# Kernel tuning notes

Measured on AMD Instinct MI355X. Metric: run time of the kernel, lower is better.

## Reference

```python
import jax, jax.numpy as jnp
import numpy as np

L = 2          # n_layer
H = 8          # n_head
DM = 512       # d_model
DFF = 2048     # d_ff
DH = DM // H   # head dim (query_dimensions)
M = DH         # Favor n_dims random features
B, S = 1, 2048
EPS = 1e-6     # causal linear attention eps
LN_EPS = 1e-5  # torch LayerNorm default


def setup_inputs() -> dict:
    key = jax.random.key(0)
    ks = jax.random.split(key, 12)
    sc = 0.02
    d = {}
    d['x'] = jax.random.normal(ks[0], (B, S, DM), dtype=jnp.float32)
    for i, (n, shape) in enumerate([('Wq', (L, DM, DM)), ('Wk', (L, DM, DM)),
                                    ('Wv', (L, DM, DM)), ('Wo', (L, DM, DM)),
                                    ('W1', (L, DM, DFF)), ('W2', (L, DFF, DM))]):
        d[n] = jax.random.normal(ks[i + 1], shape, dtype=jnp.float32) * sc
    d['bq'] = jnp.zeros((L, DM), jnp.float32)
    d['bk'] = jnp.zeros((L, DM), jnp.float32)
    d['bv'] = jnp.zeros((L, DM), jnp.float32)
    d['bo'] = jnp.zeros((L, DM), jnp.float32)
    d['b1'] = jnp.zeros((L, DFF), jnp.float32)
    d['b2'] = jnp.zeros((L, DM), jnp.float32)
    d['g1'] = jnp.ones((L, DM), jnp.float32)
    d['be1'] = jnp.zeros((L, DM), jnp.float32)
    d['g2'] = jnp.ones((L, DM), jnp.float32)
    d['be2'] = jnp.zeros((L, DM), jnp.float32)
    # FAVOR+ random projection matrix per layer: [Dh, M]
    d['omega'] = jax.random.normal(ks[7], (L, DH, M), dtype=jnp.float32)
    return d


def _favor(x, omega):
    # x: [B,S,H,Dh]; softmax_temp = 1/sqrt(Dh) applied as x * sqrt(temp)
    xs = x * (DH ** -0.25)
    nrm = jnp.sum(xs * xs, axis=-1, keepdims=True)       # [B,S,H,1]
    u = jnp.einsum('bshd,dm->bshm', xs, omega)           # [B,S,H,M]
    return jnp.exp(u - 0.5 * nrm) * (M ** -0.5)


def _ln(x, g, b):
    mu = jnp.mean(x, -1, keepdims=True)
    var = jnp.mean((x - mu) ** 2, -1, keepdims=True)
    return (x - mu) * jax.lax.rsqrt(var + LN_EPS) * g + b


def _forward(x, Wq, bq, Wk, bk, Wv, bv, Wo, bo, omega,
             W1, b1, W2, b2, g1, be1, g2, be2):
    out = x
    for l in range(L):
        q = (out @ Wq[l] + bq[l]).reshape(B, S, H, DH)
        k = (out @ Wk[l] + bk[l]).reshape(B, S, H, DH)
        v = (out @ Wv[l] + bv[l]).reshape(B, S, H, DH)
        pq = _favor(q, omega[l])
        pk = _favor(k, omega[l])
        # causal linear attention: running sums of phi(k) v^T and phi(k)
        kv = jnp.cumsum(jnp.einsum('bshm,bshd->bshmd', pk, v), axis=1)  # [B,S,H,M,Dh]
        num = jnp.einsum('bshm,bshmd->bshd', pq, kv)
        den = jnp.einsum('bshm,bshm->bsh', pq, jnp.cumsum(pk, axis=1)) + EPS
        a = (num / den[..., None]).reshape(B, S, DM)
        # post-norm encoder layer (fast-transformers TransformerEncoderLayer)
        out = out + (a @ Wo[l] + bo[l])
        out = _ln(out, g1[l], be1[l])
        y = jax.nn.relu(out @ W1[l] + b1[l]) @ W2[l] + b2[l]
        out = _ln(out + y, g2[l], be2[l])
    return out


def reference(x, Wq, bq, Wk, bk, Wv, bv, Wo, bo, omega,
              W1, b1, W2, b2, g1, be1, g2, be2):
    return _forward(x, Wq, bq, Wk, bk, Wv, bv, Wo, bo, omega,
                    W1, b1, W2, b2, g1, be1, g2, be2)
```

## Files before the change

### kernel.cpp

```cpp
#include <hip/hip_runtime.h>
#include <hip/hip_bf16.h>

#define S_  2048
#define DM_ 512
#define H_  8
#define DH_ 64
#define MF_ 64
#define DFF_ 2048
#define L_  2
#define CT_ 64
#define NC_ (S_ / CT_)
#define EPS_ 1e-6f
#define LN_EPS_ 1e-5f

#define LSW_   3145728
#define W1OFF_ 1048576
#define W2OFF_ 2097152
#define WOOFF_ 786432

typedef unsigned short ushortT;
typedef unsigned int u32;
typedef float f4 __attribute__((ext_vector_type(4)));
typedef short s8 __attribute__((ext_vector_type(8)));
typedef u32 u32x2 __attribute__((ext_vector_type(2)));

__device__ __forceinline__ ushortT f2b(float f) {
  union { float f; unsigned u; } v; v.f = f;
  unsigned r = v.u + 0x7fffu + ((v.u >> 16) & 1u);
  return (ushortT)(r >> 16);
}
__device__ __forceinline__ float bu2f(ushortT h) {
  union { unsigned u; float f; } v; v.u = ((unsigned)h) << 16; return v.f;
}
__device__ __forceinline__ u32 pk2(float a, float b) {
  return (u32)f2b(a) | ((u32)f2b(b) << 16);
}

__global__ __launch_bounds__(256) void tcast_all(
    const float* __restrict__ x,
    const float* __restrict__ Wq, const float* __restrict__ Wk,
    const float* __restrict__ Wv, const float* __restrict__ Wo,
    const float* __restrict__ W1, const float* __restrict__ W2,
    const float* __restrict__ omg,
    float* __restrict__ cur, ushortT* __restrict__ curb,
    ushortT* __restrict__ wb, ushortT* __restrict__ omgTb) {
  const int bid = blockIdx.x;
  const int t = threadIdx.x;
  if (bid >= 6152) {
    const int i = (bid - 6152) * 256 + t;
    float v = x[i];
    cur[i] = v;
    curb[i] = f2b(v);
    return;
  }
  __shared__ ushortT tile[32][33];
  const float* src; ushortT* dst; int K, N, bx, by;
  if (bid < 2048) {
    const int z = bid >> 8, widx = z & 3, lay = z >> 2;
    const float* s4[4] = {Wq, Wk, Wv, Wo};
    src = s4[widx] + (size_t)lay * DM_ * DM_;
    dst = wb + (size_t)lay * LSW_ + (size_t)widx * DM_ * DM_;
    K = DM_; N = DM_; bx = bid & 15; by = (bid >> 4) & 15;
  } else if (bid < 4096) {
    const int r = bid - 2048;
    const int lay = r >> 10;
    src = W1 + (size_t)lay * DM_ * DFF_;
    dst = wb + (size_t)lay * LSW_ + W1OFF_;
    K = DM_; N = DFF_; bx = r & 63; by = (r >> 6) & 15;
  } else if (bid < 6144) {
    const int r = bid - 4096;
    const int lay = r >> 10;
    src = W2 + (size_t)lay * DFF_ * DM_;
    dst = wb + (size_t)lay * LSW_ + W2OFF_;
    K = DFF_; N = DM_; bx = r & 15; by = (r >> 4) & 63;
  } else {
    const int r = bid - 6144;
    const int lay = r >> 2;
    src = omg + (size_t)lay * DH_ * MF_;
    dst = omgTb + (size_t)lay * DH_ * MF_;
    K = DH_; N = MF_; bx = r & 1; by = (r >> 1) & 1;
  }
  const int cc = t & 31, r0 = t >> 5;
  const int n0 = bx * 32, k0 = by * 32;
#pragma unroll
  for (int i = 0; i < 4; ++i) {
    int r = r0 + 8 * i;
    tile[r][cc] = f2b(src[(size_t)(k0 + r) * N + n0 + cc]);
  }
  __syncthreads();
#pragma unroll
  for (int i = 0; i < 4; ++i) {
    int r = r0 + 8 * i;
    dst[(size_t)(n0 + r) * K + k0 + cc] = tile[cc][r];
  }
}

template<bool OUT_BF16>
__global__ __launch_bounds__(256) void mgemm(
    const ushortT* __restrict__ A, const ushortT* __restrict__ Wt,
    const float* __restrict__ bq_, const float* __restrict__ bk_,
    const float* __restrict__ bv_,
    float* __restrict__ Cf, ushortT* __restrict__ Cb, int K, int N) {
  __shared__ ushortT sA[2][2048];
  __shared__ ushortT sB[2][2048];
  const int t = threadIdx.x;
  const int w = t >> 6, l = t & 63;
  const int wm = w >> 1, wn = w & 1;
  const int n0 = blockIdx.x * 64, m0 = blockIdx.y * 64;
  const int z = blockIdx.z;
  const ushortT* Wz = Wt + (size_t)z * K * N;
  const float* bias = (z == 0) ? bq_ : (z == 1 ? bk_ : bv_);

  const int rs = w * 16 + (l >> 2);
  const int qs = (l & 3) ^ ((rs >> 1) & 3);
  const ushortT* gA = A  + (size_t)(m0 + rs) * K + qs * 8;
  const ushortT* gB = Wz + (size_t)(n0 + rs) * K + qs * 8;

  const int Ra = wm * 32 + (l & 15);
  const int Rb = wn * 32 + (l & 15);
  const int qq = l >> 4;
  const int aoff = (Ra * 4 + (qq ^ ((Ra >> 1) & 3))) * 8;
  const int boff = (Rb * 4 + (qq ^ ((Rb >> 1) & 3))) * 8;

  f4 acc[2][2];
#pragma unroll
  for (int i = 0; i < 2; ++i)
#pragma unroll
    for (int j = 0; j < 2; ++j) acc[i][j] = (f4){0.f, 0.f, 0.f, 0.f};

  auto stage = [&](int buf, int ko) {
    __builtin_amdgcn_global_load_lds(
        (const __attribute__((address_space(1))) void*)(gA + ko),
        (__attribute__((address_space(3))) void*)(&sA[buf][w * 512]), 16, 0, 0);
    __builtin_amdgcn_global_load_lds(
        (const __attribute__((address_space(1))) void*)(gB + ko),
        (__attribute__((address_space(3))) void*)(&sB[buf][w * 512]), 16, 0, 0);
  };

  stage(0, 0);
  const int nk = K >> 5;
  for (int ks = 0; ks < nk; ++ks) {
    __syncthreads();
    if (ks + 1 < nk) stage((ks + 1) & 1, (ks + 1) * 32);
    const ushortT* pa = sA[ks & 1];
    const ushortT* pb = sB[ks & 1];
    s8 a0 = *(const s8*)(pa + aoff);
    s8 a1 = *(const s8*)(pa + aoff + 512);
    s8 b0 = *(const s8*)(pb + boff);
    s8 b1 = *(const s8*)(pb + boff + 512);
    acc[0][0] = __builtin_amdgcn_mfma_f32_16x16x32_bf16(a0, b0, acc[0][0], 0, 0, 0);
    acc[0][1] = __builtin_amdgcn_mfma_f32_16x16x32_bf16(a0, b1, acc[0][1], 0, 0, 0);
    acc[1][0] = __builtin_amdgcn_mfma_f32_16x16x32_bf16(a1, b0, acc[1][0], 0, 0, 0);
    acc[1][1] = __builtin_amdgcn_mfma_f32_16x16x32_bf16(a1, b1, acc[1][1], 0, 0, 0);
  }

  const size_t outz = (size_t)z * S_ * N;
  const int colb = n0 + wn * 32 + (l & 15);
  const int rowb = m0 + wm * 32 + ((l >> 4) << 2);
#pragma unroll
  for (int mt = 0; mt < 2; ++mt) {
#pragma unroll
    for (int nt = 0; nt < 2; ++nt) {
      const int c = colb + nt * 16;
      const float bv = bias[c];
#pragma unroll
      for (int r = 0; r < 4; ++r) {
        const int rr = rowb + mt * 16 + r;
        float v = acc[mt][nt][r] + bv;
        if (OUT_BF16) Cb[outz + (size_t)rr * N + c] = f2b(v);
        else          Cf[outz + (size_t)rr * N + c] = v;
      }
    }
  }
}

__global__ __launch_bounds__(256) void mgemm_part(
    const ushortT* __restrict__ A, const ushortT* __restrict__ Wt,
    float* __restrict__ PS, int K, int N, int KS) {
  __shared__ ushortT sA[2][2048];
  __shared__ ushortT sB[2][2048];
  const int t = threadIdx.x;
  const int w = t >> 6, l = t & 63;
  const int wm = w >> 1, wn = w & 1;
  const int n0 = blockIdx.x * 64, m0 = blockIdx.y * 64;
  const int z = blockIdx.z;

  const int rs = w * 16 + (l >> 2);
  const int qs = (l & 3) ^ ((rs >> 1) & 3);
  const ushortT* gA = A  + (size_t)(m0 + rs) * K + z * KS + qs * 8;
  const ushortT* gB = Wt + (size_t)(n0 + rs) * K + z * KS + qs * 8;

  const int Ra = wm * 32 + (l & 15);
  const int Rb = wn * 32 + (l & 15);
  const int qq = l >> 4;
  const int aoff = (Ra * 4 + (qq ^ ((Ra >> 1) & 3))) * 8;
  const int boff = (Rb * 4 + (qq ^ ((Rb >> 1) & 3))) * 8;

  f4 acc[2][2];
#pragma unroll
  for (int i = 0; i < 2; ++i)
#pragma unroll
    for (int j = 0; j < 2; ++j) acc[i][j] = (f4){0.f, 0.f, 0.f, 0.f};

  auto stage = [&](int buf, int ko) {
    __builtin_amdgcn_global_load_lds(
        (const __attribute__((address_space(1))) void*)(gA + ko),
        (__attribute__((address_space(3))) void*)(&sA[buf][w * 512]), 16, 0, 0);
    __builtin_amdgcn_global_load_lds(
        (const __attribute__((address_space(1))) void*)(gB + ko),
        (__attribute__((address_space(3))) void*)(&sB[buf][w * 512]), 16, 0, 0);
  };

  stage(0, 0);
  const int nk = KS >> 5;
  for (int ks = 0; ks < nk; ++ks) {
    __syncthreads();
    if (ks + 1 < nk) stage((ks + 1) & 1, (ks + 1) * 32);
    const ushortT* pa = sA[ks & 1];
    const ushortT* pb = sB[ks & 1];
    s8 a0 = *(const s8*)(pa + aoff);
    s8 a1 = *(const s8*)(pa + aoff + 512);
    s8 b0 = *(const s8*)(pb + boff);
    s8 b1 = *(const s8*)(pb + boff + 512);
    acc[0][0] = __builtin_amdgcn_mfma_f32_16x16x32_bf16(a0, b0, acc[0][0], 0, 0, 0);
    acc[0][1] = __builtin_amdgcn_mfma_f32_16x16x32_bf16(a0, b1, acc[0][1], 0, 0, 0);
    acc[1][0] = __builtin_amdgcn_mfma_f32_16x16x32_bf16(a1, b0, acc[1][0], 0, 0, 0);
    acc[1][1] = __builtin_amdgcn_mfma_f32_16x16x32_bf16(a1, b1, acc[1][1], 0, 0, 0);
  }

  float* out = PS + (size_t)z * S_ * N;
  const int colb = n0 + wn * 32 + (l & 15);
  const int rowb = m0 + wm * 32 + ((l >> 4) << 2);
#pragma unroll
  for (int mt = 0; mt < 2; ++mt) {
#pragma unroll
    for (int nt = 0; nt < 2; ++nt) {
      const int c = colb + nt * 16;
#pragma unroll
      for (int r = 0; r < 4; ++r)
        out[(size_t)(rowb + mt * 16 + r) * N + c] = acc[mt][nt][r];
    }
  }
}

template<bool FULL>
__global__ __launch_bounds__(256) void mgemm128(
    const ushortT* __restrict__ A, const ushortT* __restrict__ Wt,
    const float* __restrict__ bias, float* __restrict__ PS,
    ushortT* __restrict__ Cb, int K, int N, int KS) {
  __shared__ ushortT sA[2][4096];
  __shared__ ushortT sB[2][4096];
  const int t = threadIdx.x;
  const int w = t >> 6, l = t & 63, lr = l & 15, q = l >> 4;
  const int wm = w >> 1, wn = w & 1;
  const int n0 = blockIdx.x * 128, m0 = blockIdx.y * 128;
  const int z = blockIdx.z;

  const int s0 = w * 128 + l, s1 = s0 + 64;
  const int r0 = s0 >> 2, kq0 = (s0 & 3) ^ ((r0 >> 1) & 3);
  const int r1 = s1 >> 2, kq1 = (s1 & 3) ^ ((r1 >> 1) & 3);
  const ushortT* gA0 = A  + (size_t)(m0 + r0) * K + z * KS + kq0 * 8;
  const ushortT* gA1 = A  + (size_t)(m0 + r1) * K + z * KS + kq1 * 8;
  const ushortT* gB0 = Wt + (size_t)(n0 + r0) * K + z * KS + kq0 * 8;
  const ushortT* gB1 = Wt + (size_t)(n0 + r1) * K + z * KS + kq1 * 8;

  int aoff[4], boff[4];
#pragma unroll
  for (int i = 0; i < 4; ++i) {
    const int RA = wm * 64 + i * 16 + lr;
    const int RB = wn * 64 + i * 16 + lr;
    aoff[i] = (RA * 4 + (q ^ ((RA >> 1) & 3))) * 8;
    boff[i] = (RB * 4 + (q ^ ((RB >> 1) & 3))) * 8;
  }

  f4 acc[4][4];
#pragma unroll
  for (int i = 0; i < 4; ++i)
#pragma unroll
    for (int j = 0; j < 4; ++j) acc[i][j] = (f4){0.f, 0.f, 0.f, 0.f};

  auto stage = [&](int buf, int ko) {
    __builtin_amdgcn_global_load_lds(
        (const __attribute__((address_space(1))) void*)(gA0 + ko),
        (__attribute__((address_space(3))) void*)(&sA[buf][w * 1024]), 16, 0, 0);
    __builtin_amdgcn_global_load_lds(
        (const __attribute__((address_space(1))) void*)(gA1 + ko),
        (__attribute__((address_space(3))) void*)(&sA[buf][w * 1024 + 512]), 16, 0, 0);
    __builtin_amdgcn_global_load_lds(
        (const __attribute__((address_space(1))) void*)(gB0 + ko),
        (__attribute__((address_space(3))) void*)(&sB[buf][w * 1024]), 16, 0, 0);
    __builtin_amdgcn_global_load_lds(
        (const __attribute__((address_space(1))) void*)(gB1 + ko),
        (__attribute__((address_space(3))) void*)(&sB[buf][w * 1024 + 512]), 16, 0, 0);
  };

  stage(0, 0);
  const int nk = (FULL ? K : KS) >> 5;
  for (int ks = 0; ks < nk; ++ks) {
    __syncthreads();
    if (ks + 1 < nk) stage((ks + 1) & 1, (ks + 1) * 32);
    const ushortT* pa = sA[ks & 1];
    const ushortT* pb = sB[ks & 1];
    s8 a[4], b[4];
#pragma unroll
    for (int i = 0; i < 4; ++i) {
      a[i] = *(const s8*)(pa + aoff[i]);
      b[i] = *(const s8*)(pb + boff[i]);
    }
#pragma unroll
    for (int mt = 0; mt < 4; ++mt)
#pragma unroll
      for (int nt = 0; nt < 4; ++nt)
        acc[mt][nt] = __builtin_amdgcn_mfma_f32_16x16x32_bf16(a[mt], b[nt], acc[mt][nt], 0, 0, 0);
  }

  const int colb = n0 + wn * 64 + lr;
  const int rowb = m0 + wm * 64 + q * 4;
  if (FULL) {
#pragma unroll
    for (int nt = 0; nt < 4; ++nt) {
      const int c = colb + nt * 16;
      const float bv = bias[c];
#pragma unroll
      for (int mt = 0; mt < 4; ++mt) {
#pragma unroll
        for (int r = 0; r < 4; ++r) {
          const int rr = rowb + mt * 16 + r;
          Cb[(size_t)rr * N + c] = f2b(fmaxf(acc[mt][nt][r] + bv, 0.f));
        }
      }
    }
  } else {
    float* out = PS + (size_t)z * S_ * N;
#pragma unroll
    for (int mt = 0; mt < 4; ++mt)
#pragma unroll
      for (int nt = 0; nt < 4; ++nt) {
        const int c = colb + nt * 16;
#pragma unroll
        for (int r = 0; r < 4; ++r)
          out[(size_t)(rowb + mt * 16 + r) * N + c] = acc[mt][nt][r];
      }
  }
}

__global__ __launch_bounds__(256) void redln(const float* __restrict__ PS, int nsplit,
                                             const float* __restrict__ bias,
                                             const float* __restrict__ res,
                                             const float* __restrict__ g,
                                             const float* __restrict__ be,
                                             float* __restrict__ outF,
                                             ushortT* __restrict__ outB) {
  const int s = blockIdx.x, t = threadIdx.x;
  float v0 = bias[t] + res[(size_t)s * DM_ + t];
  float v1 = bias[t + 256] + res[(size_t)s * DM_ + 256 + t];
  for (int z = 0; z < nsplit; ++z) {
    const float* p = PS + (size_t)z * S_ * DM_ + (size_t)s * DM_;
    v0 += p[t];
    v1 += p[256 + t];
  }
  float sum = v0 + v1, sq = v0 * v0 + v1 * v1;
  for (int off = 32; off > 0; off >>= 1) {
    sum += __shfl_down(sum, off);
    sq += __shfl_down(sq, off);
  }
  __shared__ float ssum[4], ssq[4];
  __shared__ float smean, srstd;
  const int w = t >> 6;
  if ((t & 63) == 0) { ssum[w] = sum; ssq[w] = sq; }
  __syncthreads();
  if (t == 0) {
    float S1 = ssum[0] + ssum[1] + ssum[2] + ssum[3];
    float S2 = ssq[0] + ssq[1] + ssq[2] + ssq[3];
    float mu = S1 / DM_;
    smean = mu;
    srstd = rsqrtf(S2 / DM_ - mu * mu + LN_EPS_);
  }
  __syncthreads();
  const float mu = smean, rs = srstd;
  float o0 = (v0 - mu) * rs * g[t] + be[t];
  float o1 = (v1 - mu) * rs * g[256 + t] + be[256 + t];
  outF[(size_t)s * DM_ + t] = o0;
  outF[(size_t)s * DM_ + 256 + t] = o1;
  if (outB) {
    outB[(size_t)s * DM_ + t] = f2b(o0);
    outB[(size_t)s * DM_ + 256 + t] = f2b(o1);
  }
}

__global__ __launch_bounds__(256) void favor_cs(const ushortT* __restrict__ qkv,
                                                const ushortT* __restrict__ omgT,
                                                ushortT* __restrict__ PQb,
                                                ushortT* __restrict__ PKb,
                                                float* __restrict__ KVcT,
                                                float* __restrict__ Kc) {
  const int c = blockIdx.x, h = blockIdx.y, t = threadIdx.x;
  const int w = t >> 6, l = t & 63, lr = l & 15, q = l >> 4;
  __shared__ ushortT xq[64 * 72], xk[64 * 72], vT[64 * 72], omT[64 * 72];
  __shared__ ushortT pq[64 * 72], pk[64 * 72], pkT[64 * 72];
  __shared__ float nrm[128];

  const ushortT* qg = qkv + (size_t)(c * CT_) * DM_ + h * DH_;
  const ushortT* kg = qg + (size_t)S_ * DM_;
  const ushortT* vg = kg + (size_t)S_ * DM_;

  for (int i = t; i < 512; i += 256) {
    const int s = i >> 3, seg = i & 7;
    *(s8*)&xq[s * 72 + seg * 8] = *(const s8*)(qg + (size_t)s * DM_ + seg * 8);
    *(s8*)&xk[s * 72 + seg * 8] = *(const s8*)(kg + (size_t)s * DM_ + seg * 8);
    s8 av = *(const s8*)(vg + (size_t)s * DM_ + seg * 8);
#pragma unroll
    for (int j = 0; j < 8; ++j) vT[(seg * 8 + j) * 72 + s] = (ushortT)av[j];
    *(s8*)&omT[s * 72 + seg * 8] = *(const s8*)(omgT + s * 64 + seg * 8);
  }
  __syncthreads();

  if (t < 128) {
    const ushortT* src = (t < 64) ? xq : xk;
    const int s = t & 63;
    float a = 0.f;
#pragma unroll
    for (int seg = 0; seg < 8; ++seg) {
      s8 vv = *(const s8*)(src + s * 72 + seg * 8);
#pragma unroll
      for (int j = 0; j < 8; ++j) {
        float f = bu2f((ushortT)vv[j]);
        a += f * f;
      }
    }
    nrm[t] = a;
  }
  __syncthreads();

  {
    const float gam = 0.35355339059327373f;
    const int s0 = w * 16;
    s8 aq0 = *(const s8*)&xq[(s0 + lr) * 72 + q * 8];
    s8 aq1 = *(const s8*)&xq[(s0 + lr) * 72 + 32 + q * 8];
    s8 ak0 = *(const s8*)&xk[(s0 + lr) * 72 + q * 8];
    s8 ak1 = *(const s8*)&xk[(s0 + lr) * 72 + 32 + q * 8];
#pragma unroll
    for (int mt = 0; mt < 4; ++mt) {
      s8 b0 = *(const s8*)&omT[(mt * 16 + lr) * 72 + q * 8];
      s8 b1 = *(const s8*)&omT[(mt * 16 + lr) * 72 + 32 + q * 8];
      f4 cq = (f4){0.f, 0.f, 0.f, 0.f}, ck = (f4){0.f, 0.f, 0.f, 0.f};
      cq = __builtin_amdgcn_mfma_f32_16x16x32_bf16(aq0, b0, cq, 0, 0, 0);
      cq = __builtin_amdgcn_mfma_f32_16x16x32_bf16(aq1, b1, cq, 0, 0, 0);
      ck = __builtin_amdgcn_mfma_f32_16x16x32_bf16(ak0, b0, ck, 0, 0, 0);
      ck = __builtin_amdgcn_mfma_f32_16x16x32_bf16(ak1, b1, ck, 0, 0, 0);
#pragma unroll
      for (int r = 0; r < 4; ++r) {
        const int sr = s0 + q * 4 + r, mc = mt * 16 + lr;
        float vq = expf(gam * cq[r] - 0.0625f * nrm[sr]) * 0.125f;
        float vk = expf(gam * ck[r] - 0.0625f * nrm[64 + sr]) * 0.125f;
        pq[sr * 72 + mc] = f2b(vq);
        ushortT hk = f2b(vk);
        pk[sr * 72 + mc] = hk;
        pkT[mc * 72 + sr] = hk;
      }
    }
  }
  __syncthreads();

  {
    const int d0 = w * 16;
    s8 a0 = *(const s8*)&vT[(d0 + lr) * 72 + q * 8];
    s8 a1 = *(const s8*)&vT[(d0 + lr) * 72 + 32 + q * 8];
    float* outb = KVcT + (size_t)(h * NC_ + c) * DH_ * MF_;
#pragma unroll
    for (int mt = 0; mt < 4; ++mt) {
      s8 b0 = *(const s8*)&pkT[(mt * 16 + lr) * 72 + q * 8];
      s8 b1 = *(const s8*)&pkT[(mt * 16 + lr) * 72 + 32 + q * 8];
      f4 cc = (f4){0.f, 0.f, 0.f, 0.f};
      cc = __builtin_amdgcn_mfma_f32_16x16x32_bf16(a0, b0, cc, 0, 0, 0);
      cc = __builtin_amdgcn_mfma_f32_16x16x32_bf16(a1, b1, cc, 0, 0, 0);
#pragma unroll
      for (int r = 0; r < 4; ++r)
        outb[(size_t)(d0 + q * 4 + r) * MF_ + mt * 16 + lr] = cc[r];
    }
  }
  if (t < 64) {
    float s = 0.f;
#pragma unroll
    for (int seg = 0; seg < 8; ++seg) {
      s8 vv = *(const s8*)&pkT[t * 72 + seg * 8];
#pragma unroll
      for (int j = 0; j < 8; ++j) s += bu2f((ushortT)vv[j]);
    }
    Kc[(size_t)(h * NC_ + c) * MF_ + t] = s;
  }
  for (int i = t; i < 512; i += 256) {
    const int s = i >> 3, seg = i & 7;
    *(s8*)(PQb + (size_t)(c * CT_ + s) * DM_ + h * MF_ + seg * 8) = *(const s8*)&pq[s * 72 + seg * 8];
    *(s8*)(PKb + (size_t)(c * CT_ + s) * DM_ + h * MF_ + seg * 8) = *(const s8*)&pk[s * 72 + seg * 8];
  }
}

__global__ __launch_bounds__(256) void prefix2(float* __restrict__ KVc,
                                               float* __restrict__ Kc) {
  const int h = blockIdx.x, seg = blockIdx.y, t = threadIdx.x;
  if (seg < 16) {
    float* base = KVc + (size_t)h * NC_ * MF_ * DH_ + seg * 256 + t;
    float v[NC_];
#pragma unroll
    for (int c = 0; c < NC_; ++c) v[c] = base[(size_t)c * MF_ * DH_];
    float run = 0.f;
#pragma unroll
    for (int c = 0; c < NC_; ++c) {
      float tmp = v[c];
      base[(size_t)c * MF_ * DH_] = run;
      run += tmp;
    }
  } else if (t < MF_) {
    float* base = Kc + (size_t)h * NC_ * MF_ + t;
    float v[NC_];
#pragma unroll
    for (int c = 0; c < NC_; ++c) v[c] = base[(size_t)c * MF_];
    float run = 0.f;
#pragma unroll
    for (int c = 0; c < NC_; ++c) {
      float tmp = v[c];
      base[(size_t)c * MF_] = run;
      run += tmp;
    }
  }
}

__global__ __launch_bounds__(256) void attn_mfma(const ushortT* __restrict__ PQ,
                                                 const ushortT* __restrict__ PK,
                                                 const ushortT* __restrict__ V,
                                                 const float* __restrict__ KVcT,
                                                 const float* __restrict__ Kc,
                                                 ushortT* __restrict__ Aout) {
  const int cc = blockIdx.x, h = blockIdx.y, t = threadIdx.x;
  const int w = t >> 6, l = t & 63;
  const int lr = l & 15, q = l >> 4;

  __shared__ ushortT pqs[64 * 72];
  __shared__ ushortT pks[64 * 72];
  __shared__ ushortT vts[64 * 72];
  __shared__ ushortT kvs[64 * 72];
  __shared__ ushortT tms[64 * 72];
  __shared__ float dpart[256];
  __shared__ float den[64];

  for (int i = t; i < 512; i += 256) {
    const int s = i >> 3, seg = i & 7;
    *(s8*)&pqs[s * 72 + seg * 8] = *(const s8*)(PQ + (size_t)(cc * CT_ + s) * DM_ + h * MF_ + seg * 8);
    *(s8*)&pks[s * 72 + seg * 8] = *(const s8*)(PK + (size_t)(cc * CT_ + s) * DM_ + h * MF_ + seg * 8);
    s8 av = *(const s8*)(V + (size_t)(cc * CT_ + s) * DM_ + h * DH_ + seg * 8);
#pragma unroll
    for (int j = 0; j < 8; ++j) vts[(seg * 8 + j) * 72 + s] = (ushortT)av[j];
    const float* kr = KVcT + (size_t)((h * NC_ + cc) * DH_ + s) * MF_ + seg * 8;
    f4 g0 = *(const f4*)kr;
    f4 g1 = *(const f4*)(kr + 4);
    u32* p = (u32*)&kvs[s * 72 + seg * 8];
    p[0] = pk2(g0.x, g0.y); p[1] = pk2(g0.z, g0.w);
    p[2] = pk2(g1.x, g1.y); p[3] = pk2(g1.z, g1.w);
  }
  __syncthreads();

  {
    const int s0 = w * 16;
    s8 a0 = *(const s8*)&pqs[(s0 + lr) * 72 + q * 8];
    s8 a1 = *(const s8*)&pqs[(s0 + lr) * 72 + 32 + q * 8];
#pragma unroll
    for (int tb = 0; tb < 4; ++tb) {
      f4 c = (f4){0.f, 0.f, 0.f, 0.f};
      if (tb <= w) {
        s8 b0 = *(const s8*)&pks[(tb * 16 + lr) * 72 + q * 8];
        s8 b1 = *(const s8*)&pks[(tb * 16 + lr) * 72 + 32 + q * 8];
        c = __builtin_amdgcn_mfma_f32_16x16x32_bf16(a0, b0, c, 0, 0, 0);
        c = __builtin_amdgcn_mfma_f32_16x16x32_bf16(a1, b1, c, 0, 0, 0);
      }
#pragma unroll
      for (int r = 0; r < 4; ++r) {
        float v = c[r];
        if (tb == w && lr > q * 4 + r) v = 0.f;
        tms[(s0 + q * 4 + r) * 72 + tb * 16 + lr] = f2b(v);
      }
    }
  }
  __syncthreads();

  {
    const int s = t >> 2, part = t & 3;
    float dp = 0.f;
    const u32* trow = (const u32*)&tms[s * 72 + part * 16];
#pragma unroll
    for (int j = 0; j < 8; ++j) {
      u32 u = trow[j];
      dp += bu2f((ushortT)(u & 0xffffu)) + bu2f((ushortT)(u >> 16));
    }
    const u32* qrow = (const u32*)&pqs[s * 72 + part * 16];
    const f4* kc4 = (const f4*)(Kc + (size_t)(h * NC_ + cc) * MF_ + part * 16);
#pragma unroll
    for (int j = 0; j < 4; ++j) {
      f4 b = kc4[j];
      u32 ua = qrow[2 * j], ub = qrow[2 * j + 1];
      dp += bu2f((ushortT)(ua & 0xffffu)) * b.x + bu2f((ushortT)(ua >> 16)) * b.y +
            bu2f((ushortT)(ub & 0xffffu)) * b.z + bu2f((ushortT)(ub >> 16)) * b.w;
    }
    dpart[t] = dp;
  }
  __syncthreads();
  if (t < 64)
    den[t] = dpart[4 * t] + dpart[4 * t + 1] + dpart[4 * t + 2] + dpart[4 * t + 3] + EPS_;
  __syncthreads();

  {
    const int d0 = w * 16;
    const int drow = d0 + lr;
    s8 akv0 = *(const s8*)&kvs[drow * 72 + q * 8];
    s8 akv1 = *(const s8*)&kvs[drow * 72 + 32 + q * 8];
    s8 av0  = *(const s8*)&vts[drow * 72 + q * 8];
    s8 av1  = *(const s8*)&vts[drow * 72 + 32 + q * 8];
#pragma unroll
    for (int sb = 0; sb < 4; ++sb) {
      const int srow = sb * 16 + lr;
      s8 bq0 = *(const s8*)&pqs[srow * 72 + q * 8];
      s8 bq1 = *(const s8*)&pqs[srow * 72 + 32 + q * 8];
      s8 bt0 = *(const s8*)&tms[srow * 72 + q * 8];
      s8 bt1 = *(const s8*)&tms[srow * 72 + 32 + q * 8];
      f4 c = (f4){0.f, 0.f, 0.f, 0.f};
      c = __builtin_amdgcn_mfma_f32_16x16x32_bf16(akv0, bq0, c, 0, 0, 0);
      c = __builtin_amdgcn_mfma_f32_16x16x32_bf16(akv1, bq1, c, 0, 0, 0);
      c = __builtin_amdgcn_mfma_f32_16x16x32_bf16(av0, bt0, c, 0, 0, 0);
      c = __builtin_amdgcn_mfma_f32_16x16x32_bf16(av1, bt1, c, 0, 0, 0);
      const float inv = 1.f / den[srow];
      u32x2 o;
      o.x = pk2(c[0] * inv, c[1] * inv);
      o.y = pk2(c[2] * inv, c[3] * inv);
      *(u32x2*)(Aout + (size_t)(cc * CT_ + srow) * DM_ + h * DH_ + d0 + q * 4) = o;
    }
  }
}

extern "C" void kernel_launch(void* const* d_in, const int* in_sizes, int n_in,
                              void* d_out, int out_size, void* d_ws, size_t ws_size,
                              hipStream_t stream) {
  const float* x    = (const float*)d_in[0];
  const float* Wq   = (const float*)d_in[1];
  const float* Wk   = (const float*)d_in[2];
  const float* Wv   = (const float*)d_in[3];
  const float* Wo   = (const float*)d_in[4];
  const float* W1   = (const float*)d_in[5];
  const float* W2   = (const float*)d_in[6];
  const float* bq   = (const float*)d_in[7];
  const float* bk   = (const float*)d_in[8];
  const float* bv   = (const float*)d_in[9];
  const float* bo   = (const float*)d_in[10];
  const float* b1   = (const float*)d_in[11];
  const float* b2   = (const float*)d_in[12];
  const float* g1   = (const float*)d_in[13];
  const float* be1  = (const float*)d_in[14];
  const float* g2   = (const float*)d_in[15];
  const float* be2  = (const float*)d_in[16];
  const float* omg  = (const float*)d_in[17];
  float* out = (float*)d_out;

  const size_t MB = 1048576;
  float* f    = (float*)d_ws;
  float* cur  = f;
  float* ln1  = f + 1 * MB;
  float* KVcb = f + 2 * MB;
  float* Kcb  = f + 3 * MB;
  float* PS   = f + 3 * MB + 16384;

  ushortT* u    = (ushortT*)(f + 8 * MB);
  ushortT* curb = u;
  ushortT* qkb  = u + 1 * MB;
  ushortT* pqb  = u + 4 * MB;
  ushortT* pkb  = u + 5 * MB;
  ushortT* qbb  = u + 6 * MB;
  ushortT* ln1b = u + 7 * MB;
  ushortT* ffb  = u + 8 * MB;
  ushortT* wb   = u + 12 * MB;
  ushortT* omgTb = wb + 2 * LSW_;

  tcast_all<<<10248, 256, 0, stream>>>(x, Wq, Wk, Wv, Wo, W1, W2, omg,
                                       cur, curb, wb, omgTb);

  const dim3 gQKV(DM_ / 64, S_ / 64, 3);
  const dim3 gWo(DM_ / 64, S_ / 64, 2);
  const dim3 gW1(DFF_ / 128, S_ / 128, 1);
  const dim3 gW2(DM_ / 128, S_ / 128, 4);
  const dim3 gAttn(NC_, H_);
  const dim3 gPre(H_, 17);

  for (int l = 0; l < L_; ++l) {
    const ushortT* wl = wb + (size_t)l * LSW_;
    const size_t bo512 = (size_t)l * DM_;
    const size_t boFF = (size_t)l * DFF_;

    mgemm<true><<<gQKV, 256, 0, stream>>>(
        curb, wl, bq + bo512, bk + bo512, bv + bo512, nullptr, qkb, DM_, DM_);

    favor_cs<<<gAttn, 256, 0, stream>>>(qkb, omgTb + (size_t)l * DH_ * MF_,
                                        pqb, pkb, KVcb, Kcb);
    prefix2<<<gPre, 256, 0, stream>>>(KVcb, Kcb);
    attn_mfma<<<gAttn, 256, 0, stream>>>(pqb, pkb, qkb + 2 * (size_t)S_ * DM_,
                                         KVcb, Kcb, qbb);

    mgemm_part<<<gWo, 256, 0, stream>>>(qbb, wl + WOOFF_, PS, DM_, DM_, 256);
    redln<<<S_, 256, 0, stream>>>(PS, 2, bo + bo512, cur, g1 + bo512, be1 + bo512, ln1, ln1b);

    mgemm128<true><<<gW1, 256, 0, stream>>>(
        ln1b, wl + W1OFF_, b1 + boFF, nullptr, ffb, DM_, DFF_, 0);

    mgemm128<false><<<gW2, 256, 0, stream>>>(
        ffb, wl + W2OFF_, nullptr, PS, nullptr, DFF_, DM_, 512);
    const bool last = (l == L_ - 1);
    redln<<<S_, 256, 0, stream>>>(PS, 4, b2 + bo512, ln1, g2 + bo512, be2 + bo512,
                                  last ? out : cur, last ? nullptr : curb);
  }
}
```

Before: 249.5 us.

## Split favor and attention kernels across a z-dimension and vectorize weight transpose-cast

The FAVOR feature-map kernel now runs Q and K in separate blocks along blockIdx.z, with only the K block computing the chunk KV and K-sum state. The attention kernel is split in two along the head dimension, each block producing 32 output columns. This doubles the block count from 256 to 512 per kernel to raise occupancy on the many-CU device, at the cost of redundant loads of PQ/PK and recomputed denominators. The transpose-cast kernel also switches to float4 reads and 4-wide bf16 writes.

```diff
diff --git a/kernel.cpp b/kernel.cpp
--- a/kernel.cpp
+++ b/kernel.cpp
@@ -23,6 +23,7 @@
 typedef float f4 __attribute__((ext_vector_type(4)));
 typedef short s8 __attribute__((ext_vector_type(8)));
 typedef u32 u32x2 __attribute__((ext_vector_type(2)));
+typedef ushortT us4 __attribute__((ext_vector_type(4)));
 
 __device__ __forceinline__ ushortT f2b(float f) {
   union { float f; unsigned u; } v; v.f = f;
@@ -80,18 +81,24 @@
     dst = omgTb + (size_t)lay * DH_ * MF_;
     K = DH_; N = MF_; bx = r & 1; by = (r >> 1) & 1;
   }
-  const int cc = t & 31, r0 = t >> 5;
   const int n0 = bx * 32, k0 = by * 32;
-#pragma unroll
-  for (int i = 0; i < 4; ++i) {
-    int r = r0 + 8 * i;
-    tile[r][cc] = f2b(src[(size_t)(k0 + r) * N + n0 + cc]);
-  }
-  __syncthreads();
-#pragma unroll
-  for (int i = 0; i < 4; ++i) {
-    int r = r0 + 8 * i;
-    dst[(size_t)(n0 + r) * K + k0 + cc] = tile[cc][r];
+  {
+    const int c4 = t & 7, rl = t >> 3;
+    f4 v = *(const f4*)(src + (size_t)(k0 + rl) * N + n0 + c4 * 4);
+    tile[rl][c4 * 4 + 0] = f2b(v.x);
+    tile[rl][c4 * 4 + 1] = f2b(v.y);
+    tile[rl][c4 * 4 + 2] = f2b(v.z);
+    tile[rl][c4 * 4 + 3] = f2b(v.w);
+  }
+  __syncthreads();
+  {
+    const int cs = t & 7, rs = t >> 3;
+    us4 o;
+    o.x = tile[cs * 4 + 0][rs];
+    o.y = tile[cs * 4 + 1][rs];
+    o.z = tile[cs * 4 + 2][rs];
+    o.w = tile[cs * 4 + 3][rs];
+    *(us4*)(dst + (size_t)(n0 + rs) * K + k0 + cs * 4) = o;
   }
 }
 
@@ -388,40 +395,41 @@
   }
 }
 
-__global__ __launch_bounds__(256) void favor_cs(const ushortT* __restrict__ qkv,
+__global__ __launch_bounds__(256) void favor_sp(const ushortT* __restrict__ qkv,
                                                 const ushortT* __restrict__ omgT,
                                                 ushortT* __restrict__ PQb,
                                                 ushortT* __restrict__ PKb,
                                                 float* __restrict__ KVcT,
                                                 float* __restrict__ Kc) {
-  const int c = blockIdx.x, h = blockIdx.y, t = threadIdx.x;
+  const int c = blockIdx.x, h = blockIdx.y, z = blockIdx.z, t = threadIdx.x;
   const int w = t >> 6, l = t & 63, lr = l & 15, q = l >> 4;
-  __shared__ ushortT xq[64 * 72], xk[64 * 72], vT[64 * 72], omT[64 * 72];
-  __shared__ ushortT pq[64 * 72], pk[64 * 72], pkT[64 * 72];
-  __shared__ float nrm[128];
-
-  const ushortT* qg = qkv + (size_t)(c * CT_) * DM_ + h * DH_;
-  const ushortT* kg = qg + (size_t)S_ * DM_;
-  const ushortT* vg = kg + (size_t)S_ * DM_;
+  __shared__ ushortT xx[64 * 72];
+  __shared__ ushortT vT[64 * 72];
+  __shared__ ushortT omT[64 * 72];
+  __shared__ ushortT pp[64 * 72];
+  __shared__ ushortT ppT[64 * 72];
+  __shared__ float nrm[64];
+
+  const ushortT* xg = qkv + (z ? (size_t)S_ * DM_ : 0) + (size_t)(c * CT_) * DM_ + h * DH_;
+  const ushortT* vg = qkv + 2 * (size_t)S_ * DM_ + (size_t)(c * CT_) * DM_ + h * DH_;
 
   for (int i = t; i < 512; i += 256) {
     const int s = i >> 3, seg = i & 7;
-    *(s8*)&xq[s * 72 + seg * 8] = *(const s8*)(qg + (size_t)s * DM_ + seg * 8);
-    *(s8*)&xk[s * 72 + seg * 8] = *(const s8*)(kg + (size_t)s * DM_ + seg * 8);
-    s8 av = *(const s8*)(vg + (size_t)s * DM_ + seg * 8);
-#pragma unroll
-    for (int j = 0; j < 8; ++j) vT[(seg * 8 + j) * 72 + s] = (ushortT)av[j];
+    *(s8*)&xx[s * 72 + seg * 8] = *(const s8*)(xg + (size_t)s * DM_ + seg * 8);
     *(s8*)&omT[s * 72 + seg * 8] = *(const s8*)(omgT + s * 64 + seg * 8);
-  }
-  __syncthreads();
-
-  if (t < 128) {
-    const ushortT* src = (t < 64) ? xq : xk;
-    const int s = t & 63;
+    if (z) {
+      s8 av = *(const s8*)(vg + (size_t)s * DM_ + seg * 8);
+#pragma unroll
+      for (int j = 0; j < 8; ++j) vT[(seg * 8 + j) * 72 + s] = (ushortT)av[j];
+    }
+  }
+  __syncthreads();
+
+  if (t < 64) {
     float a = 0.f;
 #pragma unroll
     for (int seg = 0; seg < 8; ++seg) {
-      s8 vv = *(const s8*)(src + s * 72 + seg * 8);
+      s8 vv = *(const s8*)(xx + t * 72 + seg * 8);
 #pragma unroll
       for (int j = 0; j < 8; ++j) {
         float f = bu2f((ushortT)vv[j]);
@@ -435,64 +443,58 @@
   {
     const float gam = 0.35355339059327373f;
     const int s0 = w * 16;
-    s8 aq0 = *(const s8*)&xq[(s0 + lr) * 72 + q * 8];
-    s8 aq1 = *(const s8*)&xq[(s0 + lr) * 72 + 32 + q * 8];
-    s8 ak0 = *(const s8*)&xk[(s0 + lr) * 72 + q * 8];
-    s8 ak1 = *(const s8*)&xk[(s0 + lr) * 72 + 32 + q * 8];
+    s8 a0 = *(const s8*)&xx[(s0 + lr) * 72 + q * 8];
+    s8 a1 = *(const s8*)&xx[(s0 + lr) * 72 + 32 + q * 8];
 #pragma unroll
     for (int mt = 0; mt < 4; ++mt) {
       s8 b0 = *(const s8*)&omT[(mt * 16 + lr) * 72 + q * 8];
       s8 b1 = *(const s8*)&omT[(mt * 16 + lr) * 72 + 32 + q * 8];
-      f4 cq = (f4){0.f, 0.f, 0.f, 0.f}, ck = (f4){0.f, 0.f, 0.f, 0.f};
-      cq = __builtin_amdgcn_mfma_f32_16x16x32_bf16(aq0, b0, cq, 0, 0, 0);
-      cq = __builtin_amdgcn_mfma_f32_16x16x32_bf16(aq1, b1, cq, 0, 0, 0);
-      ck = __builtin_amdgcn_mfma_f32_16x16x32_bf16(ak0, b0, ck, 0, 0, 0);
-      ck = __builtin_amdgcn_mfma_f32_16x16x32_bf16(ak1, b1, ck, 0, 0, 0);
+      f4 cu = (f4){0.f, 0.f, 0.f, 0.f};
+      cu = __builtin_amdgcn_mfma_f32_16x16x32_bf16(a0, b0, cu, 0, 0, 0);
+      cu = __builtin_amdgcn_mfma_f32_16x16x32_bf16(a1, b1, cu, 0, 0, 0);
 #pragma unroll
       for (int r = 0; r < 4; ++r) {
         const int sr = s0 + q * 4 + r, mc = mt * 16 + lr;
-        float vq = expf(gam * cq[r] - 0.0625f * nrm[sr]) * 0.125f;
-        float vk = expf(gam * ck[r] - 0.0625f * nrm[64 + sr]) * 0.125f;
-        pq[sr * 72 + mc] = f2b(vq);
-        ushortT hk = f2b(vk);
-        pk[sr * 72 + mc] = hk;
-        pkT[mc * 72 + sr] = hk;
+        float v = expf(gam * cu[r] - 0.0625f * nrm[sr]) * 0.125f;
+        ushortT hv = f2b(v);
+        pp[sr * 72 + mc] = hv;
+        if (z) ppT[mc * 72 + sr] = hv;
       }
     }
   }
   __syncthreads();
 
-  {
+  if (z) {
     const int d0 = w * 16;
     s8 a0 = *(const s8*)&vT[(d0 + lr) * 72 + q * 8];
     s8 a1 = *(const s8*)&vT[(d0 + lr) * 72 + 32 + q * 8];
     float* outb = KVcT + (size_t)(h * NC_ + c) * DH_ * MF_;
 #pragma unroll
     for (int mt = 0; mt < 4; ++mt) {
-      s8 b0 = *(const s8*)&pkT[(mt * 16 + lr) * 72 + q * 8];
-      s8 b1 = *(const s8*)&pkT[(mt * 16 + lr) * 72 + 32 + q * 8];
-      f4 cc = (f4){0.f, 0.f, 0.f, 0.f};
-      cc = __builtin_amdgcn_mfma_f32_16x16x32_bf16(a0, b0, cc, 0, 0, 0);
-      cc = __builtin_amdgcn_mfma_f32_16x16x32_bf16(a1, b1, cc, 0, 0, 0);
+      s8 b0 = *(const s8*)&ppT[(mt * 16 + lr) * 72 + q * 8];
+      s8 b1 = *(const s8*)&ppT[(mt * 16 + lr) * 72 + 32 + q * 8];
+      f4 cs = (f4){0.f, 0.f, 0.f, 0.f};
+      cs = __builtin_amdgcn_mfma_f32_16x16x32_bf16(a0, b0, cs, 0, 0, 0);
+      cs = __builtin_amdgcn_mfma_f32_16x16x32_bf16(a1, b1, cs, 0, 0, 0);
 #pragma unroll
       for (int r = 0; r < 4; ++r)
-        outb[(size_t)(d0 + q * 4 + r) * MF_ + mt * 16 + lr] = cc[r];
-    }
-  }
-  if (t < 64) {
-    float s = 0.f;
-#pragma unroll
-    for (int seg = 0; seg < 8; ++seg) {
-      s8 vv = *(const s8*)&pkT[t * 72 + seg * 8];
-#pragma unroll
-      for (int j = 0; j < 8; ++j) s += bu2f((ushortT)vv[j]);
-    }
-    Kc[(size_t)(h * NC_ + c) * MF_ + t] = s;
-  }
+        outb[(size_t)(d0 + q * 4 + r) * MF_ + mt * 16 + lr] = cs[r];
+    }
+    if (t < 64) {
+      float s = 0.f;
+#pragma unroll
+      for (int seg = 0; seg < 8; ++seg) {
+        s8 vv = *(const s8*)&ppT[t * 72 + seg * 8];
+#pragma unroll
+        for (int j = 0; j < 8; ++j) s += bu2f((ushortT)vv[j]);
+      }
+      Kc[(size_t)(h * NC_ + c) * MF_ + t] = s;
+    }
+  }
+  ushortT* dst = z ? PKb : PQb;
   for (int i = t; i < 512; i += 256) {
     const int s = i >> 3, seg = i & 7;
-    *(s8*)(PQb + (size_t)(c * CT_ + s) * DM_ + h * MF_ + seg * 8) = *(const s8*)&pq[s * 72 + seg * 8];
-    *(s8*)(PKb + (size_t)(c * CT_ + s) * DM_ + h * MF_ + seg * 8) = *(const s8*)&pk[s * 72 + seg * 8];
+    *(s8*)(dst + (size_t)(c * CT_ + s) * DM_ + h * MF_ + seg * 8) = *(const s8*)&pp[s * 72 + seg * 8];
   }
 }
 
@@ -526,21 +528,21 @@
   }
 }
 
-__global__ __launch_bounds__(256) void attn_mfma(const ushortT* __restrict__ PQ,
-                                                 const ushortT* __restrict__ PK,
-                                                 const ushortT* __restrict__ V,
-                                                 const float* __restrict__ KVcT,
-                                                 const float* __restrict__ Kc,
-                                                 ushortT* __restrict__ Aout) {
-  const int cc = blockIdx.x, h = blockIdx.y, t = threadIdx.x;
+__global__ __launch_bounds__(256) void attn_sp(const ushortT* __restrict__ PQ,
+                                               const ushortT* __restrict__ PK,
+                                               const ushortT* __restrict__ V,
+                                               const float* __restrict__ KVcT,
+                                               const float* __restrict__ Kc,
+                                               ushortT* __restrict__ Aout) {
+  const int cc = blockIdx.x, h = blockIdx.y, z = blockIdx.z, t = threadIdx.x;
   const int w = t >> 6, l = t & 63;
   const int lr = l & 15, q = l >> 4;
 
   __shared__ ushortT pqs[64 * 72];
   __shared__ ushortT pks[64 * 72];
-  __shared__ ushortT vts[64 * 72];
-  __shared__ ushortT kvs[64 * 72];
   __shared__ ushortT tms[64 * 72];
+  __shared__ ushortT vts[32 * 72];
+  __shared__ ushortT kvs[32 * 72];
   __shared__ float dpart[256];
   __shared__ float den[64];
 
@@ -548,13 +550,19 @@
     const int s = i >> 3, seg = i & 7;
     *(s8*)&pqs[s * 72 + seg * 8] = *(const s8*)(PQ + (size_t)(cc * CT_ + s) * DM_ + h * MF_ + seg * 8);
     *(s8*)&pks[s * 72 + seg * 8] = *(const s8*)(PK + (size_t)(cc * CT_ + s) * DM_ + h * MF_ + seg * 8);
+  }
+  {
+    const int s = t >> 2, segl = t & 3, seg = z * 4 + segl;
     s8 av = *(const s8*)(V + (size_t)(cc * CT_ + s) * DM_ + h * DH_ + seg * 8);
 #pragma unroll
-    for (int j = 0; j < 8; ++j) vts[(seg * 8 + j) * 72 + s] = (ushortT)av[j];
-    const float* kr = KVcT + (size_t)((h * NC_ + cc) * DH_ + s) * MF_ + seg * 8;
+    for (int j = 0; j < 8; ++j) vts[(segl * 8 + j) * 72 + s] = (ushortT)av[j];
+  }
+  {
+    const int dl = t >> 3, seg = t & 7;
+    const float* kr = KVcT + (size_t)((h * NC_ + cc) * DH_ + z * 32 + dl) * MF_ + seg * 8;
     f4 g0 = *(const f4*)kr;
     f4 g1 = *(const f4*)(kr + 4);
-    u32* p = (u32*)&kvs[s * 72 + seg * 8];
+    u32* p = (u32*)&kvs[dl * 72 + seg * 8];
     p[0] = pk2(g0.x, g0.y); p[1] = pk2(g0.z, g0.w);
     p[2] = pk2(g1.x, g1.y); p[3] = pk2(g1.z, g1.w);
   }
@@ -609,14 +617,16 @@
   __syncthreads();
 
   {
-    const int d0 = w * 16;
-    const int drow = d0 + lr;
-    s8 akv0 = *(const s8*)&kvs[drow * 72 + q * 8];
-    s8 akv1 = *(const s8*)&kvs[drow * 72 + 32 + q * 8];
-    s8 av0  = *(const s8*)&vts[drow * 72 + q * 8];
-    s8 av1  = *(const s8*)&vts[drow * 72 + 32 + q * 8];
-#pragma unroll
-    for (int sb = 0; sb < 4; ++sb) {
+    const int dgrp = w & 1, sbh = w >> 1;
+    const int dl = dgrp * 16 + lr;
+    s8 akv0 = *(const s8*)&kvs[dl * 72 + q * 8];
+    s8 akv1 = *(const s8*)&kvs[dl * 72 + 32 + q * 8];
+    s8 av0  = *(const s8*)&vts[dl * 72 + q * 8];
+    s8 av1  = *(const s8*)&vts[dl * 72 + 32 + q * 8];
+    const int dcol = h * DH_ + z * 32 + dgrp * 16;
+#pragma unroll
+    for (int sbi = 0; sbi < 2; ++sbi) {
+      const int sb = sbh * 2 + sbi;
       const int srow = sb * 16 + lr;
       s8 bq0 = *(const s8*)&pqs[srow * 72 + q * 8];
       s8 bq1 = *(const s8*)&pqs[srow * 72 + 32 + q * 8];
@@ -631,7 +641,7 @@
       u32x2 o;
       o.x = pk2(c[0] * inv, c[1] * inv);
       o.y = pk2(c[2] * inv, c[3] * inv);
-      *(u32x2*)(Aout + (size_t)(cc * CT_ + srow) * DM_ + h * DH_ + d0 + q * 4) = o;
+      *(u32x2*)(Aout + (size_t)(cc * CT_ + srow) * DM_ + dcol + q * 4) = o;
     }
   }
 }
@@ -685,7 +695,8 @@
   const dim3 gWo(DM_ / 64, S_ / 64, 2);
   const dim3 gW1(DFF_ / 128, S_ / 128, 1);
   const dim3 gW2(DM_ / 128, S_ / 128, 4);
-  const dim3 gAttn(NC_, H_);
+  const dim3 gFav(NC_, H_, 2);
+  const dim3 gAtt(NC_, H_, 2);
   const dim3 gPre(H_, 17);
 
   for (int l = 0; l < L_; ++l) {
@@ -696,11 +707,11 @@
     mgemm<true><<<gQKV, 256, 0, stream>>>(
         curb, wl, bq + bo512, bk + bo512, bv + bo512, nullptr, qkb, DM_, DM_);
 
-    favor_cs<<<gAttn, 256, 0, stream>>>(qkb, omgTb + (size_t)l * DH_ * MF_,
-                                        pqb, pkb, KVcb, Kcb);
+    favor_sp<<<gFav, 256, 0, stream>>>(qkb, omgTb + (size_t)l * DH_ * MF_,
+                                       pqb, pkb, KVcb, Kcb);
     prefix2<<<gPre, 256, 0, stream>>>(KVcb, Kcb);
-    attn_mfma<<<gAttn, 256, 0, stream>>>(pqb, pkb, qkb + 2 * (size_t)S_ * DM_,
-                                         KVcb, Kcb, qbb);
+    attn_sp<<<gAtt, 256, 0, stream>>>(pqb, pkb, qkb + 2 * (size_t)S_ * DM_,
+                                      KVcb, Kcb, qbb);
 
     mgemm_part<<<gWo, 256, 0, stream>>>(qbb, wl + WOOFF_, PS, DM_, DM_, 256);
     redln<<<S_, 256, 0, stream>>>(PS, 2, bo + bo512, cur, g1 + bo512, be1 + bo512, ln1, ln1b);
```

After: 244.6 us. About the same (-1.9%).
